# Performance work log

Measured on AMD Instinct MI355X. Metric: run time of the kernel, lower is better.

## Reference

```python
import jax, jax.numpy as jnp
import numpy as np

B, GRID, IN_CO, OUT_CO = 32, 4096, 64, 64
T_EMB, N_MODES = 256, 512
M_HALF = N_MODES // 2 + 1  # 257 retained rFFT modes


def setup_inputs() -> dict:
    key = jax.random.key(0)
    ks = jax.random.split(key, 6)
    w_std = jnp.sqrt(1.0 / (2.0 * IN_CO))
    return {
        "x": jax.random.normal(ks[0], (B, GRID, IN_CO), jnp.float32),
        "t_emb": jax.random.normal(ks[1], (B, T_EMB), jnp.float32),
        "weights_real": jax.random.normal(ks[2], (M_HALF, IN_CO, OUT_CO), jnp.float32) * w_std,
        "weights_imag": jax.random.normal(ks[3], (M_HALF, IN_CO, OUT_CO), jnp.float32) * w_std,
        "dense_real": jax.random.normal(ks[4], (T_EMB, M_HALF), jnp.float32) * jnp.sqrt(1.0 / T_EMB),
        "dense_imag": jax.random.normal(ks[5], (T_EMB, M_HALF), jnp.float32) * jnp.sqrt(1.0 / T_EMB),
    }


def reference(x, t_emb, weights_real, weights_imag, dense_real, dense_imag):
    b, in_grid_sz, _ = x.shape
    m = weights_real.shape[0]  # n_modes//2 + 1
    weights = weights_real + 1j * weights_imag  # (m, in_co, out_co)
    # rFFT over the grid axis
    x_ft = jnp.fft.rfft(x, axis=-2, norm="forward")  # (b, grid//2+1, in_co) complex
    # time modulation per mode: Dense(real) + i*Dense(imag)
    t_tr = (t_emb @ dense_real) + 1j * (t_emb @ dense_imag)  # (b, m)
    # original einsum with eye == elementwise per-mode scale then per-mode matmul
    x_out = jnp.einsum("bmi,mio->bmo", x_ft[:, :m, :], weights) * t_tr[:, :, None]
    out_ft = jnp.zeros((b, in_grid_sz // 2 + 1, weights.shape[-1]), jnp.complex64)
    out_ft = out_ft.at[:, :m, :].set(x_out)
    return jnp.fft.irfft(out_ft, axis=-2, n=in_grid_sz, norm="forward")
```

## Files before the change

kernel.cpp:

```cpp
#include <hip/hip_runtime.h>
#include <hip/hip_bf16.h>

typedef short short8 __attribute__((ext_vector_type(8)));
typedef float f32x4 __attribute__((ext_vector_type(4)));
typedef const void __attribute__((address_space(1))) as1_void;
typedef void __attribute__((address_space(3))) as3_void;

__device__ __forceinline__ float sin_rev(float r) {
  float o; asm("v_sin_f32 %0, %1" : "=v"(o) : "v"(r)); return o;
}
__device__ __forceinline__ float cos_rev(float r) {
  float o; asm("v_cos_f32 %0, %1" : "=v"(o) : "v"(r)); return o;
}

#define INV4096 0.000244140625f
#define INV16   0.0625f

__global__ __launch_bounds__(256) void prep_kernel(__hip_bfloat16* __restrict__ F2,
                                                   __hip_bfloat16* __restrict__ Gm,
                                                   const float* __restrict__ t_emb,
                                                   const float* __restrict__ dr,
                                                   const float* __restrict__ di,
                                                   float* __restrict__ Sr,
                                                   float* __restrict__ Si,
                                                   const float* __restrict__ x,
                                                   __hip_bfloat16* __restrict__ X2T,
                                                   float* __restrict__ Xr256p,
                                                   const float* __restrict__ Wr,
                                                   const float* __restrict__ Wi,
                                                   __hip_bfloat16* __restrict__ Wb) {
  const int bid = blockIdx.x;
  const int tid = threadIdx.x;
  __shared__ float te[256];
  __shared__ float tile[64][65];
  __shared__ float red[4][64];

  if (bid < 512) {
    const int row = bid;
    const int m   = (row < 256) ? row : (row - 255);
    const bool is_cos = (row < 256);
#pragma unroll
    for (int it = 0; it < 2; ++it) {
      int n0 = it * 2048 + tid * 8;
      union { short8 v; unsigned short u[8]; } pk;
#pragma unroll
      for (int j = 0; j < 8; ++j) {
        int ph = (m * (n0 + j)) & 4095;
        float v = is_cos ?  cos_rev((float)ph * INV4096)
                         : -sin_rev((float)ph * INV4096);
        __hip_bfloat16 h = __float2bfloat16(v);
        pk.u[j] = *(unsigned short*)&h;
      }
      *(short8*)&F2[(size_t)row * 4096 + n0] = pk.v;
    }
  } else if (bid < 1024) {
    const int nb = (bid - 512) * 8;
#pragma unroll
    for (int it = 0; it < 2; ++it) {
      int e  = it * 2048 + tid * 8;
      int n  = nb + (e >> 9);
      int k0 = e & 511;
      union { short8 v; unsigned short u[8]; } pk;
#pragma unroll
      for (int j = 0; j < 8; ++j) {
        int kk = k0 + j;
        int m  = (kk < 256) ? kk : (kk - 255);
        int ph = (m * n) & 4095;
        float v = (kk < 256) ?  cos_rev((float)ph * INV4096)
                             : -sin_rev((float)ph * INV4096);
        __hip_bfloat16 h = __float2bfloat16(v);
        pk.u[j] = *(unsigned short*)&h;
      }
      *(short8*)&Gm[(size_t)n * 512 + k0] = pk.v;
    }
  } else if (bid < 1056) {
    int b = bid - 1024;
    te[tid] = t_emb[b * 256 + tid];
    __syncthreads();
    for (int m = tid; m < 257; m += 256) {
      float ar = 0.f, ai = 0.f;
      for (int t = 0; t < 256; ++t) {
        float e = te[t];
        ar += e * dr[t * 257 + m];
        ai += e * di[t * 257 + m];
      }
      float c = (m == 0 ? 1.0f : 2.0f) * (1.0f / 4096.0f);
      Sr[b * 257 + m] = ar * c;
      Si[b * 257 + m] = ai * c;
    }
  } else if (bid < 3104) {
    int idx = bid - 1056;
    int nt = idx & 63;
    int b  = idx >> 6;
    int n0 = nt * 64;
#pragma unroll
    for (int it = 0; it < 4; ++it) {
      int c = it * 256 + tid;
      int r = c >> 4, i4 = (c & 15) * 4;
      float4 v = *(const float4*)&x[((size_t)b * 4096 + n0 + r) * 64 + i4];
      tile[r][i4 + 0] = v.x; tile[r][i4 + 1] = v.y;
      tile[r][i4 + 2] = v.z; tile[r][i4 + 3] = v.w;
    }
    __syncthreads();
#pragma unroll
    for (int it = 0; it < 2; ++it) {
      int c  = it * 256 + tid;
      int i  = c >> 3;
      int ch = c & 7;
      union { short8 v; unsigned short u[8]; } pk;
#pragma unroll
      for (int j = 0; j < 8; ++j) {
        __hip_bfloat16 h = __float2bfloat16(tile[ch * 8 + j][i]);
        pk.u[j] = *(unsigned short*)&h;
      }
      *(short8*)&X2T[((size_t)b * 64 + i) * 4096 + n0 + ch * 8] = pk.v;
    }
    {
      int i = tid & 63, g = tid >> 6;
      float acc = 0.f;
#pragma unroll
      for (int j = 0; j < 16; ++j)
        acc += cos_rev((float)j * INV16) * tile[g * 16 + j][i];
      red[g][i] = acc;
    }
    __syncthreads();
    if (tid < 64) {
      Xr256p[((size_t)b * 64 + nt) * 64 + tid] =
          red[0][tid] + red[1][tid] + red[2][tid] + red[3][tid];
    }
  } else {
    int idx  = bid - 3104;
    int k    = idx >> 2;
    int quad = idx & 3;
    const float* src = (quad < 2) ? (Wr + (size_t)k * 4096 + quad * 2048)
                                  : (Wi + (size_t)k * 4096 + (quad - 2) * 2048);
    __hip_bfloat16* dst = Wb + (size_t)k * 8192 + (quad < 2 ? quad * 2048 : 4096 + (quad - 2) * 2048);
    int e = tid * 8;
    float4 v0 = *(const float4*)&src[e];
    float4 v1 = *(const float4*)&src[e + 4];
    union { short8 v; unsigned short u[8]; } pk;
    float vv[8] = {v0.x, v0.y, v0.z, v0.w, v1.x, v1.y, v1.z, v1.w};
#pragma unroll
    for (int j = 0; j < 8; ++j) {
      __hip_bfloat16 h = __float2bfloat16(vv[j]);
      pk.u[j] = *(unsigned short*)&h;
    }
    *(short8*)&dst[e] = pk.v;
  }
}

template <int NF>
__device__ __forceinline__ void stage_tileT(const __hip_bfloat16* __restrict__ A, int lda, int m0,
                                            const __hip_bfloat16* __restrict__ B, int ldb, int n0,
                                            int kt, __hip_bfloat16* As, __hip_bfloat16* Bs,
                                            int tid) {
#pragma unroll
  for (int j = 0; j < 4; ++j) {
    int c   = j * 256 + tid;
    int row = c >> 3;
    int chg = (c & 7) ^ (row & 7);
    const __hip_bfloat16* ga = A + (size_t)(m0 + row) * lda + kt + chg * 8;
    __hip_bfloat16* la = As + (size_t)(j * 256 + (tid & 192)) * 8;
    __builtin_amdgcn_global_load_lds((as1_void*)ga, (as3_void*)la, 16, 0, 0);
  }
#pragma unroll
  for (int j = 0; j < NF; ++j) {
    int c   = j * 256 + tid;
    int row = c >> 3;
    int chg = (c & 7) ^ (row & 7);
    const __hip_bfloat16* gb = B + (size_t)(n0 + row) * ldb + kt + chg * 8;
    __hip_bfloat16* lb = Bs + (size_t)(j * 256 + (tid & 192)) * 8;
    __builtin_amdgcn_global_load_lds((as1_void*)gb, (as3_void*)lb, 16, 0, 0);
  }
}

template <int NF>
__device__ __forceinline__ void compute_stepT(const __hip_bfloat16* As, const __hip_bfloat16* Bs,
                                              int wr, int wc, int fr, int fq,
                                              f32x4 acc[4][NF]) {
#pragma unroll
  for (int kk = 0; kk < 2; ++kk) {
    short8 av[4], bv[NF];
#pragma unroll
    for (int m = 0; m < 4; ++m) {
      int row  = wr + m * 16 + fr;
      int slot = (fq + kk * 4) ^ (row & 7);
      av[m] = *(const short8*)(As + row * 64 + slot * 8);
    }
#pragma unroll
    for (int n = 0; n < NF; ++n) {
      int row  = wc + n * 16 + fr;
      int slot = (fq + kk * 4) ^ (row & 7);
      bv[n] = *(const short8*)(Bs + row * 64 + slot * 8);
    }
#pragma unroll
    for (int m = 0; m < 4; ++m)
#pragma unroll
      for (int n = 0; n < NF; ++n)
        acc[m][n] = __builtin_amdgcn_mfma_f32_16x16x32_bf16(av[m], bv[n], acc[m][n], 0, 0, 0);
  }
}

template <int NF>
__device__ __forceinline__ void gemm_coreT(const __hip_bfloat16* __restrict__ A, int lda, int m0,
                                           const __hip_bfloat16* __restrict__ B, int ldb, int n0,
                                           int k0, int ksteps,
                                           __hip_bfloat16* As, __hip_bfloat16* Bs,
                                           f32x4 acc[4][NF]) {
  const int tid  = threadIdx.x;
  const int lane = tid & 63;
  const int wv   = tid >> 6;
  const int wr   = (wv >> 1) * 64;
  const int wc   = (wv & 1) * (NF * 16);
  const int fr   = lane & 15;
  const int fq   = lane >> 4;

  for (int ks = 0; ks < ksteps; ++ks) {
    stage_tileT<NF>(A, lda, m0, B, ldb, n0, k0 + ks * 64, As, Bs, tid);
    __syncthreads();
    compute_stepT<NF>(As, Bs, wr, wc, fr, fq, acc);
    __syncthreads();
  }
}

__global__ __launch_bounds__(256) void gemm1_kernel(const __hip_bfloat16* __restrict__ F2,
                                                    const __hip_bfloat16* __restrict__ X2T,
                                                    __hip_bfloat16* __restrict__ C1, int kchunk) {
  __shared__ __hip_bfloat16 As[128 * 64];
  __shared__ __hip_bfloat16 Bs[128 * 64];
  int n0 = blockIdx.x * 128;
  int m0 = blockIdx.y * 128;
  int k0 = blockIdx.z * kchunk;
  f32x4 acc[4][4];
#pragma unroll
  for (int m = 0; m < 4; ++m)
#pragma unroll
    for (int n = 0; n < 4; ++n)
#pragma unroll
      for (int r = 0; r < 4; ++r) acc[m][n][r] = 0.f;

  gemm_coreT<4>(F2, 4096, m0, X2T, 4096, n0, k0, kchunk >> 6, As, Bs, acc);

  const int lane = threadIdx.x & 63;
  const int wv   = threadIdx.x >> 6;
  const int wr   = (wv >> 1) * 64, wc = (wv & 1) * 64;
  const int fr   = lane & 15, fq = lane >> 4;
  __hip_bfloat16* P = C1 + (size_t)blockIdx.z * (512 * 2048);
#pragma unroll
  for (int m = 0; m < 4; ++m)
#pragma unroll
    for (int n = 0; n < 4; ++n)
#pragma unroll
      for (int j = 0; j < 4; ++j) {
        int row = m0 + wr + m * 16 + fq * 4 + j;
        int col = n0 + wc + n * 16 + fr;
        P[(size_t)row * 2048 + col] = __float2bfloat16(acc[m][n][j]);
      }
}

__global__ __launch_bounds__(256) void mix_kernel(const __hip_bfloat16* __restrict__ C1,
                                                  const float* __restrict__ Xr256p,
                                                  const __hip_bfloat16* __restrict__ Wb,
                                                  const float* __restrict__ Sr,
                                                  const float* __restrict__ Si,
                                                  __hip_bfloat16* __restrict__ Y2T,
                                                  __hip_bfloat16* __restrict__ Yx,
                                                  int splitk) {
  const int k = blockIdx.x;
  const int q = blockIdx.y;
  const int tid = threadIdx.x;
  __shared__ float wlr[4096];
  __shared__ float wli[4096];
  __shared__ float xs2[2][1024];
  __shared__ float xs[1024];

  const __hip_bfloat16* wbg = Wb + (size_t)k * 8192;
  for (int c = tid; c < 1024; c += 256) {
    short8 v = *(const short8*)(wbg + c * 8);
    float* dst = (c < 512) ? &wlr[c * 8] : &wli[(c - 512) * 8];
#pragma unroll
    for (int j = 0; j < 8; ++j) {
      unsigned short u = (unsigned short)v[j];
      dst[j] = __bfloat162float(*(__hip_bfloat16*)&u);
    }
  }

  const size_t PST = 512ull * 2048;
  if (k < 256) {
    const int zg   = tid >> 7;
    const int part = (tid >> 6) & 1;
    const int ln   = tid & 63;
    const int row  = (part == 0) ? k : 255 + k;
    float f[8] = {0.f, 0.f, 0.f, 0.f, 0.f, 0.f, 0.f, 0.f};
    if (part == 0 || k > 0) {
      const __hip_bfloat16* src = C1 + (size_t)row * 2048 + q * 512 + ln * 8;
      const int zh = splitk >> 1;
      for (int z = zg * zh; z < zg * zh + zh; ++z) {
        short8 v = *(const short8*)(src + (size_t)z * PST);
#pragma unroll
        for (int j = 0; j < 8; ++j) {
          unsigned short u = (unsigned short)v[j];
          f[j] += __bfloat162float(*(__hip_bfloat16*)&u);
        }
      }
    }
#pragma unroll
    for (int j = 0; j < 8; ++j) xs2[zg][part * 512 + ln * 8 + j] = f[j];
    __syncthreads();
    for (int e = tid; e < 1024; e += 256) xs[e] = xs2[0][e] + xs2[1][e];
  } else {
    for (int idx = tid; idx < 1024; idx += 256) {
      int part = idx >> 9;
      int c    = idx & 511;
      float s = 0.f;
      if (part == 0) {
        int bi = q * 512 + c;
        const float* sp = Xr256p + (size_t)(bi >> 6) * 4096 + (bi & 63);
#pragma unroll 8
        for (int nt = 0; nt < 64; ++nt) s += sp[nt * 64];
      } else {
        const __hip_bfloat16* src = C1 + (size_t)511 * 2048 + q * 512 + c;
        for (int z = 0; z < splitk; ++z) s += __bfloat162float(src[(size_t)z * PST]);
      }
      xs[idx] = s;
    }
    __syncthreads();
  }
  __syncthreads();

  const int o  = tid & 63;
  const int jj = tid >> 6;
  const int bl0 = jj * 2, bl1 = jj * 2 + 1;
  float pr0 = 0.f, pi0 = 0.f, pr1 = 0.f, pi1 = 0.f;
#pragma unroll 8
  for (int i = 0; i < 64; ++i) {
    float wrv = wlr[i * 64 + o];
    float wiv = wli[i * 64 + o];
    float xr0 = xs[bl0 * 64 + i], xi0 = xs[512 + bl0 * 64 + i];
    float xr1 = xs[bl1 * 64 + i], xi1 = xs[512 + bl1 * 64 + i];
    pr0 += xr0 * wrv - xi0 * wiv;
    pi0 += xr0 * wiv + xi0 * wrv;
    pr1 += xr1 * wrv - xi1 * wiv;
    pi1 += xr1 * wiv + xi1 * wrv;
  }
  int b0 = q * 8 + bl0, b1 = q * 8 + bl1;
  float sr0 = Sr[b0 * 257 + k], si0 = Si[b0 * 257 + k];
  float sr1 = Sr[b1 * 257 + k], si1 = Si[b1 * 257 + k];
  int bo0 = b0 * 64 + o, bo1 = b1 * 64 + o;
  __hip_bfloat16 yr0 = __float2bfloat16(pr0 * sr0 - pi0 * si0);
  __hip_bfloat16 yi0 = __float2bfloat16(pr0 * si0 + pi0 * sr0);
  __hip_bfloat16 yr1 = __float2bfloat16(pr1 * sr1 - pi1 * si1);
  __hip_bfloat16 yi1 = __float2bfloat16(pr1 * si1 + pi1 * sr1);
  if (k < 256) {
    Y2T[(size_t)bo0 * 512 + k] = yr0;
    Y2T[(size_t)bo1 * 512 + k] = yr1;
  } else {
    Yx[bo0] = yr0;
    Yx[bo1] = yr1;
  }
  if (k >= 1) {
    Y2T[(size_t)bo0 * 512 + 255 + k] = yi0;
    Y2T[(size_t)bo1 * 512 + 255 + k] = yi1;
  }
}

__global__ __launch_bounds__(256) void gemm2_kernel(const __hip_bfloat16* __restrict__ Gm,
                                                    const __hip_bfloat16* __restrict__ Y2T,
                                                    const __hip_bfloat16* __restrict__ Yx,
                                                    float* __restrict__ out) {
  __shared__ __hip_bfloat16 As[128 * 64];
  __shared__ __hip_bfloat16 Bs[64 * 64];
  int n0 = blockIdx.x * 64;
  int m0 = blockIdx.y * 128;
  f32x4 acc[4][2];
#pragma unroll
  for (int m = 0; m < 4; ++m)
#pragma unroll
    for (int n = 0; n < 2; ++n)
#pragma unroll
      for (int r = 0; r < 4; ++r) acc[m][n][r] = 0.f;

  gemm_coreT<2>(Gm, 512, m0, Y2T, 512, n0, 0, 8, As, Bs, acc);

  const int lane = threadIdx.x & 63;
  const int wv   = threadIdx.x >> 6;
  const int wr   = (wv >> 1) * 64, wc = (wv & 1) * 32;
  const int fr   = lane & 15, fq = lane >> 4;
  float yx[2];
#pragma unroll
  for (int n = 0; n < 2; ++n)
    yx[n] = __bfloat162float(Yx[n0 + wc + n * 16 + fr]);
#pragma unroll
  for (int m = 0; m < 4; ++m)
#pragma unroll
    for (int j = 0; j < 4; ++j) {
      int row = m0 + wr + m * 16 + fq * 4 + j;
      float g = cos_rev((float)(row & 15) * INV16);
#pragma unroll
      for (int n = 0; n < 2; ++n) {
        int col = n0 + wc + n * 16 + fr;
        int b = col >> 6, o = col & 63;
        out[((size_t)b * 4096 + row) * 64 + o] = acc[m][n][j] + g * yx[n];
      }
    }
}

extern "C" void kernel_launch(void* const* d_in, const int* in_sizes, int n_in,
                              void* d_out, int out_size, void* d_ws, size_t ws_size,
                              hipStream_t stream) {
  const float* x  = (const float*)d_in[0];
  const float* te = (const float*)d_in[1];
  const float* wr = (const float*)d_in[2];
  const float* wi = (const float*)d_in[3];
  const float* dr = (const float*)d_in[4];
  const float* di = (const float*)d_in[5];
  float* out = (float*)d_out;

  char* p = (char*)d_ws;
  auto alloc = [&](size_t bytes) -> char* {
    char* r = p;
    p += (bytes + 255) & ~(size_t)255;
    return r;
  };
  __hip_bfloat16* F2  = (__hip_bfloat16*)alloc(512ull * 4096 * 2);
  __hip_bfloat16* Gm  = (__hip_bfloat16*)alloc(4096ull * 512 * 2);
  __hip_bfloat16* X2T = (__hip_bfloat16*)alloc(2048ull * 4096 * 2);
  float* Xr256p = (float*)alloc(32ull * 64 * 64 * 4);
  float* Sr = (float*)alloc(32 * 257 * 4);
  float* Si = (float*)alloc(32 * 257 * 4);
  __hip_bfloat16* Y2T = (__hip_bfloat16*)alloc(2048ull * 512 * 2);
  __hip_bfloat16* Yx  = (__hip_bfloat16*)alloc(2048 * 2);
  __hip_bfloat16* Wb  = (__hip_bfloat16*)alloc(257ull * 8192 * 2);
  size_t fixed = (size_t)(p - (char*)d_ws);

  int splitk = 2;
  if (ws_size >= fixed + 8ull * 512 * 2048 * 2)      splitk = 8;
  else if (ws_size >= fixed + 4ull * 512 * 2048 * 2) splitk = 4;
  __hip_bfloat16* C1 = (__hip_bfloat16*)alloc((size_t)splitk * 512 * 2048 * 2);
  int kchunk = 4096 / splitk;

  prep_kernel<<<4132, 256, 0, stream>>>(F2, Gm, te, dr, di, Sr, Si, x, X2T, Xr256p, wr, wi, Wb);
  gemm1_kernel<<<dim3(16, 4, splitk), 256, 0, stream>>>(F2, X2T, C1, kchunk);
  mix_kernel<<<dim3(257, 4), 256, 0, stream>>>(C1, Xr256p, Wb, Sr, Si, Y2T, Yx, splitk);
  gemm2_kernel<<<dim3(32, 32), 256, 0, stream>>>(Gm, Y2T, Yx, out);
}
```

Baseline: 89.72 us.

## Exploit DFT even/odd symmetry to halve forward and inverse GEMM sizes

The forward DFT now folds the grid with its mirror into even (x[n]+x[N-n]) and odd (x[n]-x[N-n]) bf16 parts. The cos rows multiply the even part and the sin rows the odd part, which halves the K dimension of gemm1. The inverse transform computes cos and sin partial sums over half the grid and writes both out[n] and out[N-n] from them. A separate path handles the n=N/2 and n=0 edge terms. This cuts GEMM FLOPs, the DFT-matrix size and the bf16 input staging traffic, at the cost of more index bookkeeping and added bf16 rounding on the summed inputs.

```diff
diff --git a/kernel.cpp b/kernel.cpp
--- a/kernel.cpp
+++ b/kernel.cpp
@@ -17,62 +17,60 @@
 #define INV16   0.0625f
 
 __global__ __launch_bounds__(256) void prep_kernel(__hip_bfloat16* __restrict__ F2,
-                                                   __hip_bfloat16* __restrict__ Gm,
+                                                   __hip_bfloat16* __restrict__ Gm2,
                                                    const float* __restrict__ t_emb,
                                                    const float* __restrict__ dr,
                                                    const float* __restrict__ di,
                                                    float* __restrict__ Sr,
                                                    float* __restrict__ Si,
                                                    const float* __restrict__ x,
-                                                   __hip_bfloat16* __restrict__ X2T,
+                                                   __hip_bfloat16* __restrict__ E,
+                                                   __hip_bfloat16* __restrict__ O,
                                                    float* __restrict__ Xr256p,
+                                                   float* __restrict__ x2048f,
                                                    const float* __restrict__ Wr,
                                                    const float* __restrict__ Wi,
                                                    __hip_bfloat16* __restrict__ Wb) {
   const int bid = blockIdx.x;
   const int tid = threadIdx.x;
   __shared__ float te[256];
-  __shared__ float tile[64][65];
+  __shared__ float tileA[64][65];
+  __shared__ float tileB[64][65];
   __shared__ float red[4][64];
+  __shared__ float xm[64];
 
   if (bid < 512) {
     const int row = bid;
     const int m   = (row < 256) ? row : (row - 255);
     const bool is_cos = (row < 256);
-#pragma unroll
-    for (int it = 0; it < 2; ++it) {
-      int n0 = it * 2048 + tid * 8;
-      union { short8 v; unsigned short u[8]; } pk;
-#pragma unroll
-      for (int j = 0; j < 8; ++j) {
-        int ph = (m * (n0 + j)) & 4095;
-        float v = is_cos ?  cos_rev((float)ph * INV4096)
-                         : -sin_rev((float)ph * INV4096);
-        __hip_bfloat16 h = __float2bfloat16(v);
-        pk.u[j] = *(unsigned short*)&h;
-      }
-      *(short8*)&F2[(size_t)row * 4096 + n0] = pk.v;
-    }
+    int n0 = tid * 8;
+    union { short8 v; unsigned short u[8]; } pk;
+#pragma unroll
+    for (int j = 0; j < 8; ++j) {
+      int ph = (m * (n0 + j)) & 4095;
+      float v = is_cos ?  cos_rev((float)ph * INV4096)
+                       : -sin_rev((float)ph * INV4096);
+      __hip_bfloat16 h = __float2bfloat16(v);
+      pk.u[j] = *(unsigned short*)&h;
+    }
+    *(short8*)&F2[(size_t)row * 2048 + n0] = pk.v;
   } else if (bid < 1024) {
-    const int nb = (bid - 512) * 8;
-#pragma unroll
-    for (int it = 0; it < 2; ++it) {
-      int e  = it * 2048 + tid * 8;
-      int n  = nb + (e >> 9);
-      int k0 = e & 511;
-      union { short8 v; unsigned short u[8]; } pk;
-#pragma unroll
-      for (int j = 0; j < 8; ++j) {
-        int kk = k0 + j;
-        int m  = (kk < 256) ? kk : (kk - 255);
-        int ph = (m * n) & 4095;
-        float v = (kk < 256) ?  cos_rev((float)ph * INV4096)
-                             : -sin_rev((float)ph * INV4096);
-        __hip_bfloat16 h = __float2bfloat16(v);
-        pk.u[j] = *(unsigned short*)&h;
-      }
-      *(short8*)&Gm[(size_t)n * 512 + k0] = pk.v;
-    }
+    const int gb = bid - 512;
+    int e  = tid * 8;
+    int n  = gb * 4 + (e >> 9);
+    int c0 = e & 511;
+    union { short8 v; unsigned short u[8]; } pk;
+#pragma unroll
+    for (int j = 0; j < 8; ++j) {
+      int cc = c0 + j;
+      int k  = (cc < 256) ? cc : (cc - 255);
+      int ph = (n * k) & 4095;
+      float v = (cc < 256) ? cos_rev((float)ph * INV4096)
+                           : sin_rev((float)ph * INV4096);
+      __hip_bfloat16 h = __float2bfloat16(v);
+      pk.u[j] = *(unsigned short*)&h;
+    }
+    *(short8*)&Gm2[(size_t)n * 512 + c0] = pk.v;
   } else if (bid < 1056) {
     int b = bid - 1024;
     te[tid] = t_emb[b * 256 + tid];
@@ -88,48 +86,63 @@
       Sr[b * 257 + m] = ar * c;
       Si[b * 257 + m] = ai * c;
     }
-  } else if (bid < 3104) {
+  } else if (bid < 2080) {
     int idx = bid - 1056;
-    int nt = idx & 63;
-    int b  = idx >> 6;
+    int nt = idx & 31;
+    int b  = idx >> 5;
     int n0 = nt * 64;
+    int m0r = (63 - nt) * 64;
 #pragma unroll
     for (int it = 0; it < 4; ++it) {
       int c = it * 256 + tid;
       int r = c >> 4, i4 = (c & 15) * 4;
       float4 v = *(const float4*)&x[((size_t)b * 4096 + n0 + r) * 64 + i4];
-      tile[r][i4 + 0] = v.x; tile[r][i4 + 1] = v.y;
-      tile[r][i4 + 2] = v.z; tile[r][i4 + 3] = v.w;
-    }
+      tileA[r][i4 + 0] = v.x; tileA[r][i4 + 1] = v.y;
+      tileA[r][i4 + 2] = v.z; tileA[r][i4 + 3] = v.w;
+      float4 w = *(const float4*)&x[((size_t)b * 4096 + m0r + r) * 64 + i4];
+      tileB[r][i4 + 0] = w.x; tileB[r][i4 + 1] = w.y;
+      tileB[r][i4 + 2] = w.z; tileB[r][i4 + 3] = w.w;
+    }
+    if (tid < 64) xm[tid] = (nt > 0) ? x[((size_t)b * 4096 + (4096 - n0)) * 64 + tid] : 0.f;
     __syncthreads();
 #pragma unroll
     for (int it = 0; it < 2; ++it) {
       int c  = it * 256 + tid;
       int i  = c >> 3;
       int ch = c & 7;
-      union { short8 v; unsigned short u[8]; } pk;
-#pragma unroll
-      for (int j = 0; j < 8; ++j) {
-        __hip_bfloat16 h = __float2bfloat16(tile[ch * 8 + j][i]);
-        pk.u[j] = *(unsigned short*)&h;
-      }
-      *(short8*)&X2T[((size_t)b * 64 + i) * 4096 + n0 + ch * 8] = pk.v;
+      union { short8 v; unsigned short u[8]; } pe, po;
+#pragma unroll
+      for (int jj = 0; jj < 8; ++jj) {
+        int j = ch * 8 + jj;
+        float a = tileA[j][i];
+        float mir = (j == 0) ? xm[i] : tileB[64 - j][i];
+        __hip_bfloat16 he = __float2bfloat16(a + mir);
+        __hip_bfloat16 ho = __float2bfloat16(a - mir);
+        pe.u[jj] = *(unsigned short*)&he;
+        po.u[jj] = *(unsigned short*)&ho;
+      }
+      size_t base = ((size_t)b * 64 + i) * 2048 + n0 + ch * 8;
+      *(short8*)&E[base] = pe.v;
+      *(short8*)&O[base] = po.v;
     }
     {
       int i = tid & 63, g = tid >> 6;
       float acc = 0.f;
 #pragma unroll
-      for (int j = 0; j < 16; ++j)
-        acc += cos_rev((float)j * INV16) * tile[g * 16 + j][i];
+      for (int j = 0; j < 16; ++j) {
+        float w = cos_rev((float)j * INV16);
+        acc += w * (tileA[g * 16 + j][i] + tileB[g * 16 + j][i]);
+      }
       red[g][i] = acc;
     }
     __syncthreads();
     if (tid < 64) {
-      Xr256p[((size_t)b * 64 + nt) * 64 + tid] =
+      Xr256p[((size_t)b * 32 + nt) * 64 + tid] =
           red[0][tid] + red[1][tid] + red[2][tid] + red[3][tid];
+      if (nt == 31) x2048f[b * 64 + tid] = tileB[0][tid];
     }
   } else {
-    int idx  = bid - 3104;
+    int idx  = bid - 2080;
     int k    = idx >> 2;
     int quad = idx & 3;
     const float* src = (quad < 2) ? (Wr + (size_t)k * 4096 + quad * 2048)
@@ -224,13 +237,15 @@
 }
 
 __global__ __launch_bounds__(256) void gemm1_kernel(const __hip_bfloat16* __restrict__ F2,
-                                                    const __hip_bfloat16* __restrict__ X2T,
+                                                    const __hip_bfloat16* __restrict__ E,
+                                                    const __hip_bfloat16* __restrict__ O,
                                                     __hip_bfloat16* __restrict__ C1, int kchunk) {
   __shared__ __hip_bfloat16 As[128 * 64];
   __shared__ __hip_bfloat16 Bs[128 * 64];
   int n0 = blockIdx.x * 128;
   int m0 = blockIdx.y * 128;
   int k0 = blockIdx.z * kchunk;
+  const __hip_bfloat16* B = (m0 < 256) ? E : O;
   f32x4 acc[4][4];
 #pragma unroll
   for (int m = 0; m < 4; ++m)
@@ -239,7 +254,7 @@
 #pragma unroll
       for (int r = 0; r < 4; ++r) acc[m][n][r] = 0.f;
 
-  gemm_coreT<4>(F2, 4096, m0, X2T, 4096, n0, k0, kchunk >> 6, As, Bs, acc);
+  gemm_coreT<4>(F2, 2048, m0, B, 2048, n0, k0, kchunk >> 6, As, Bs, acc);
 
   const int lane = threadIdx.x & 63;
   const int wv   = threadIdx.x >> 6;
@@ -260,6 +275,7 @@
 
 __global__ __launch_bounds__(256) void mix_kernel(const __hip_bfloat16* __restrict__ C1,
                                                   const float* __restrict__ Xr256p,
+                                                  const float* __restrict__ x2048f,
                                                   const __hip_bfloat16* __restrict__ Wb,
                                                   const float* __restrict__ Sr,
                                                   const float* __restrict__ Si,
@@ -304,6 +320,11 @@
         }
       }
     }
+    if (part == 0 && zg == 0) {
+      float par = (k & 1) ? -1.f : 1.f;
+#pragma unroll
+      for (int j = 0; j < 8; ++j) f[j] += par * x2048f[q * 512 + ln * 8 + j];
+    }
 #pragma unroll
     for (int j = 0; j < 8; ++j) xs2[zg][part * 512 + ln * 8 + j] = f[j];
     __syncthreads();
@@ -315,9 +336,9 @@
       float s = 0.f;
       if (part == 0) {
         int bi = q * 512 + c;
-        const float* sp = Xr256p + (size_t)(bi >> 6) * 4096 + (bi & 63);
+        const float* sp = Xr256p + (size_t)(bi >> 6) * 2048 + (bi & 63);
 #pragma unroll 8
-        for (int nt = 0; nt < 64; ++nt) s += sp[nt * 64];
+        for (int nt = 0; nt < 32; ++nt) s += sp[nt * 64];
       } else {
         const __hip_bfloat16* src = C1 + (size_t)511 * 2048 + q * 512 + c;
         for (int z = 0; z < splitk; ++z) s += __bfloat162float(src[(size_t)z * PST]);
@@ -364,23 +385,25 @@
   }
 }
 
-__global__ __launch_bounds__(256) void gemm2_kernel(const __hip_bfloat16* __restrict__ Gm,
+__global__ __launch_bounds__(256) void gemm2_kernel(const __hip_bfloat16* __restrict__ Gm2,
                                                     const __hip_bfloat16* __restrict__ Y2T,
                                                     const __hip_bfloat16* __restrict__ Yx,
                                                     float* __restrict__ out) {
   __shared__ __hip_bfloat16 As[128 * 64];
   __shared__ __hip_bfloat16 Bs[64 * 64];
+  __shared__ float red2[4][64];
   int n0 = blockIdx.x * 64;
   int m0 = blockIdx.y * 128;
-  f32x4 acc[4][2];
+  f32x4 accC[4][2], accS[4][2];
 #pragma unroll
   for (int m = 0; m < 4; ++m)
 #pragma unroll
     for (int n = 0; n < 2; ++n)
 #pragma unroll
-      for (int r = 0; r < 4; ++r) acc[m][n][r] = 0.f;
-
-  gemm_coreT<2>(Gm, 512, m0, Y2T, 512, n0, 0, 8, As, Bs, acc);
+      for (int r = 0; r < 4; ++r) { accC[m][n][r] = 0.f; accS[m][n][r] = 0.f; }
+
+  gemm_coreT<2>(Gm2, 512, m0, Y2T, 512, n0, 0,   4, As, Bs, accC);
+  gemm_coreT<2>(Gm2, 512, m0, Y2T, 512, n0, 256, 4, As, Bs, accS);
 
   const int lane = threadIdx.x & 63;
   const int wv   = threadIdx.x >> 6;
@@ -400,9 +423,34 @@
       for (int n = 0; n < 2; ++n) {
         int col = n0 + wc + n * 16 + fr;
         int b = col >> 6, o = col & 63;
-        out[((size_t)b * 4096 + row) * 64 + o] = acc[m][n][j] + g * yx[n];
-      }
-    }
+        float vC = accC[m][n][j] + g * yx[n];
+        float vS = accS[m][n][j];
+        out[((size_t)b * 4096 + row) * 64 + o] = vC - vS;
+        if (row > 0)
+          out[((size_t)b * 4096 + (4096 - row)) * 64 + o] = vC + vS;
+      }
+    }
+
+  if (m0 == 0) {
+    __syncthreads();
+    const int tid = threadIdx.x;
+    int col = tid & 63, grp = tid >> 6;
+    int bo = n0 + col;
+    float s = 0.f;
+    for (int k = grp * 64; k < grp * 64 + 64; ++k) {
+      float v = __bfloat162float(Y2T[(size_t)bo * 512 + k]);
+      s += (k & 1) ? -v : v;
+    }
+    red2[grp][col] = s;
+    __syncthreads();
+    if (tid < 64) {
+      int bo2 = n0 + tid;
+      float alt = red2[0][tid] + red2[1][tid] + red2[2][tid] + red2[3][tid]
+                + __bfloat162float(Yx[bo2]);
+      int b = bo2 >> 6, o = bo2 & 63;
+      out[((size_t)b * 4096 + 2048) * 64 + o] = alt;
+    }
+  }
 }
 
 extern "C" void kernel_launch(void* const* d_in, const int* in_sizes, int n_in,
@@ -422,10 +470,12 @@
     p += (bytes + 255) & ~(size_t)255;
     return r;
   };
-  __hip_bfloat16* F2  = (__hip_bfloat16*)alloc(512ull * 4096 * 2);
-  __hip_bfloat16* Gm  = (__hip_bfloat16*)alloc(4096ull * 512 * 2);
-  __hip_bfloat16* X2T = (__hip_bfloat16*)alloc(2048ull * 4096 * 2);
-  float* Xr256p = (float*)alloc(32ull * 64 * 64 * 4);
+  __hip_bfloat16* F2  = (__hip_bfloat16*)alloc(512ull * 2048 * 2);
+  __hip_bfloat16* Gm2 = (__hip_bfloat16*)alloc(2048ull * 512 * 2);
+  __hip_bfloat16* E   = (__hip_bfloat16*)alloc(2048ull * 2048 * 2);
+  __hip_bfloat16* O   = (__hip_bfloat16*)alloc(2048ull * 2048 * 2);
+  float* Xr256p = (float*)alloc(32ull * 32 * 64 * 4);
+  float* x2048f = (float*)alloc(2048 * 4);
   float* Sr = (float*)alloc(32 * 257 * 4);
   float* Si = (float*)alloc(32 * 257 * 4);
   __hip_bfloat16* Y2T = (__hip_bfloat16*)alloc(2048ull * 512 * 2);
@@ -437,10 +487,11 @@
   if (ws_size >= fixed + 8ull * 512 * 2048 * 2)      splitk = 8;
   else if (ws_size >= fixed + 4ull * 512 * 2048 * 2) splitk = 4;
   __hip_bfloat16* C1 = (__hip_bfloat16*)alloc((size_t)splitk * 512 * 2048 * 2);
-  int kchunk = 4096 / splitk;
-
-  prep_kernel<<<4132, 256, 0, stream>>>(F2, Gm, te, dr, di, Sr, Si, x, X2T, Xr256p, wr, wi, Wb);
-  gemm1_kernel<<<dim3(16, 4, splitk), 256, 0, stream>>>(F2, X2T, C1, kchunk);
-  mix_kernel<<<dim3(257, 4), 256, 0, stream>>>(C1, Xr256p, Wb, Sr, Si, Y2T, Yx, splitk);
-  gemm2_kernel<<<dim3(32, 32), 256, 0, stream>>>(Gm, Y2T, Yx, out);
-}
+  int kchunk = 2048 / splitk;
+
+  prep_kernel<<<3108, 256, 0, stream>>>(F2, Gm2, te, dr, di, Sr, Si, x, E, O,
+                                        Xr256p, x2048f, wr, wi, Wb);
+  gemm1_kernel<<<dim3(16, 4, splitk), 256, 0, stream>>>(F2, E, O, C1, kchunk);
+  mix_kernel<<<dim3(257, 4), 256, 0, stream>>>(C1, Xr256p, x2048f, Wb, Sr, Si, Y2T, Yx, splitk);
+  gemm2_kernel<<<dim3(32, 16), 256, 0, stream>>>(Gm2, Y2T, Yx, out);
+}
```

After: 88.87 us. No clear change (-0.9%).
